# Performance work log

Hardware: AMD Instinct MI355X
Metric: run time of the kernel (lower is better)

Reference implementation:

```python
import jax, jax.numpy as jnp
import numpy as np

N_NODES = 50000
N_EDGES = 800000
D = 128
L = 3


def setup_inputs() -> dict:
    key = jax.random.key(0)
    ks = jax.random.split(key, 8)
    h = jax.random.normal(ks[0], (N_NODES, D), dtype=jnp.float32)
    src = jax.random.randint(ks[1], (N_EDGES,), 0, N_NODES, dtype=jnp.int32)
    dst = jax.random.randint(ks[2], (N_EDGES,), 0, N_NODES, dtype=jnp.int32)
    # MLP weights per GIN layer, scaled ~Glorot to keep activations bounded across layers
    w_scale = 0.05
    W1 = jax.random.normal(ks[3], (L, D, D), dtype=jnp.float32) * w_scale
    b1 = jnp.zeros((L, D), dtype=jnp.float32)
    W2 = jax.random.normal(ks[4], (L, D, D), dtype=jnp.float32) * w_scale
    b2 = jnp.zeros((L, D), dtype=jnp.float32)
    eps = jnp.zeros((L,), dtype=jnp.float32)  # init_eps=0, learnable
    return {"h": h, "src": src, "dst": dst, "W1": W1, "b1": b1, "W2": W2, "b2": b2, "eps": eps}


def reference(h, src, dst, W1, b1, W2, b2, eps):
    # GIN: h <- MLP((1 + eps) * h + sum_{(u->v) in E} h_u) per layer (sum aggregation)
    n = h.shape[0]
    for l in range(W1.shape[0]):
        agg = jax.ops.segment_sum(h[src], dst, num_segments=n)  # [N, D]
        z = (1.0 + eps[l]) * h + agg
        hid = jnp.maximum(z @ W1[l] + b1[l], 0.0)  # Linear + ReLU
        h = hid @ W2[l] + b2[l]                    # Linear
    return h
```

## Files before the change

kernel.cpp:

```cpp
#include <hip/hip_runtime.h>
#include <hip/hip_bf16.h>
#include <stdint.h>

#define N_NODES 50000
#define N_EDGES 800000
#define D 128
#define NLAYER 3
#define NGROUP (N_NODES / 16)
#define CAPG 384
#define GSTRIDE 384
#define MAXCH 12

#define NBKT2 196
#define BCAP 4608
#define EPB_A 2048
#define PA_BLOCKS ((N_EDGES + EPB_A - 1) / EPB_A)

typedef __attribute__((ext_vector_type(8))) short bf16x8;
typedef __attribute__((ext_vector_type(4))) float f32x4;
typedef __attribute__((ext_vector_type(2))) float f32x2;

__device__ __forceinline__ short f2bf(float f) {
    union { float f; uint32_t u; } v; v.f = f;
    uint32_t u = v.u;
    uint32_t r = u + 0x7fffu + ((u >> 16) & 1u);
    return (short)(r >> 16);
}
__device__ __forceinline__ float bf2f(short s) {
    union { uint32_t u; float f; } v;
    v.u = ((uint32_t)(uint16_t)s) << 16;
    return v.f;
}

__device__ __forceinline__ bf16x8 f8_to_bf16x8(uint2 r) {
    f32x2 f01 = __builtin_amdgcn_cvt_pk_f32_fp8(r.x, false);
    f32x2 f23 = __builtin_amdgcn_cvt_pk_f32_fp8(r.x, true);
    f32x2 f45 = __builtin_amdgcn_cvt_pk_f32_fp8(r.y, false);
    f32x2 f67 = __builtin_amdgcn_cvt_pk_f32_fp8(r.y, true);
    uint32_t w0, w1, w2, w3;
    asm("v_cvt_pk_bf16_f32 %0, %1, %2" : "=v"(w0) : "v"(f01.x), "v"(f01.y));
    asm("v_cvt_pk_bf16_f32 %0, %1, %2" : "=v"(w1) : "v"(f23.x), "v"(f23.y));
    asm("v_cvt_pk_bf16_f32 %0, %1, %2" : "=v"(w2) : "v"(f45.x), "v"(f45.y));
    asm("v_cvt_pk_bf16_f32 %0, %1, %2" : "=v"(w3) : "v"(f67.x), "v"(f67.y));
    union { uint32_t w[4]; bf16x8 v; } u;
    u.w[0] = w0; u.w[1] = w1; u.w[2] = w2; u.w[3] = w3;
    return u.v;
}

__device__ __forceinline__ unsigned char f2fp8(float f) {
    return (unsigned char)(__builtin_amdgcn_cvt_pk_fp8_f32(f, f, 0u, false) & 0xFF);
}

__global__ void wconv(const float* __restrict__ W1, const float* __restrict__ W2,
                      short* __restrict__ Wswz) {
    int t = blockIdx.x * blockDim.x + threadIdx.x;
    if (t >= NLAYER * 2 * 4 * 8 * 64) return;
    int lane = t & 63;
    int nt   = (t >> 6) & 7;
    int ks   = (t >> 9) & 3;
    int mat  = (t >> 11) & 1;
    int l    = t >> 12;
    const float* W = (mat == 0 ? W1 : W2) + (size_t)l * D * D;
    int n = nt * 16 + (lane & 15);
    short* outp = Wswz + (size_t)t * 8;
#pragma unroll
    for (int j = 0; j < 8; ++j) {
        int k = ks * 32 + (lane >> 4) * 8 + j;
        outp[j] = f2bf(W[k * D + n]);
    }
}

__global__ void h2bf(const float* __restrict__ h, short* __restrict__ hbf,
                     unsigned char* __restrict__ hf8) {
    int t = blockIdx.x * blockDim.x + threadIdx.x;
    if (t >= N_NODES * D / 8) return;
    f32x4 a = ((const f32x4*)h)[2 * t];
    f32x4 b = ((const f32x4*)h)[2 * t + 1];
    bf16x8 o;
    o[0] = f2bf(a.x); o[1] = f2bf(a.y); o[2] = f2bf(a.z); o[3] = f2bf(a.w);
    o[4] = f2bf(b.x); o[5] = f2bf(b.y); o[6] = f2bf(b.z); o[7] = f2bf(b.w);
    ((bf16x8*)hbf)[t] = o;
    uint32_t lo = 0, hi = 0;
    lo = __builtin_amdgcn_cvt_pk_fp8_f32(a.x, a.y, lo, false);
    lo = __builtin_amdgcn_cvt_pk_fp8_f32(a.z, a.w, lo, true);
    hi = __builtin_amdgcn_cvt_pk_fp8_f32(b.x, b.y, hi, false);
    hi = __builtin_amdgcn_cvt_pk_fp8_f32(b.z, b.w, hi, true);
    ((uint2*)hf8)[t] = make_uint2(lo, hi);
}

__global__ void zero_bcur(int* __restrict__ bcur) {
    if (threadIdx.x < NBKT2) bcur[threadIdx.x] = 0;
}

__global__ __launch_bounds__(256) void packA(const int* __restrict__ src,
                                             const int* __restrict__ dst,
                                             int* __restrict__ bcur,
                                             int* __restrict__ epack) {
    __shared__ int hcnt[NBKT2];
    __shared__ int hbase[NBKT2];
    if (threadIdx.x < NBKT2) hcnt[threadIdx.x] = 0;
    __syncthreads();
    int base = blockIdx.x * EPB_A;
    int end = base + EPB_A; if (end > N_EDGES) end = N_EDGES;
    for (int e = base + threadIdx.x; e < end; e += 256)
        atomicAdd(&hcnt[dst[e] >> 8], 1);
    __syncthreads();
    if (threadIdx.x < NBKT2) {
        int c = hcnt[threadIdx.x];
        hbase[threadIdx.x] = c ? atomicAdd(&bcur[threadIdx.x], c) : 0;
        hcnt[threadIdx.x] = 0;
    }
    __syncthreads();
    for (int e = base + threadIdx.x; e < end; e += 256) {
        int s = src[e], d = dst[e];
        int b = d >> 8;
        int r = atomicAdd(&hcnt[b], 1);
        int slot = hbase[b] + r;
        if (slot < BCAP)
            epack[(size_t)b * BCAP + slot] = (s << 8) | (d & 255);
    }
}

__global__ __launch_bounds__(256) void segB(const int* __restrict__ epack,
                                            const int* __restrict__ bcur,
                                            int* __restrict__ esd,
                                            int* __restrict__ gcnt) {
    __shared__ int image[16 * GSTRIDE];
    __shared__ int cur[16];
    const int b = blockIdx.x;
    int n = bcur[b]; if (n > BCAP) n = BCAP;
    const int* ep = epack + (size_t)b * BCAP;
    const int nG = (NGROUP - b * 16 < 16) ? (NGROUP - b * 16) : 16;

    for (int i = threadIdx.x; i < 16 * GSTRIDE; i += 256) image[i] = 0x80;
    if (threadIdx.x < 16) cur[threadIdx.x] = 0;
    __syncthreads();
    for (int i = threadIdx.x; i < n; i += 256) {
        int e = ep[i];
        int g = (e >> 4) & 15;
        int r = atomicAdd(&cur[g], 1);
        if (r < CAPG) image[g * GSTRIDE + r] = e & ~0xF0;
    }
    __syncthreads();
    if (threadIdx.x < nG) {
        int c = cur[threadIdx.x];
        gcnt[b * 16 + threadIdx.x] = (c > CAPG) ? CAPG : c;
    }
    for (int i = threadIdx.x; i < nG * GSTRIDE; i += 256)
        esd[(size_t)(b * 16) * GSTRIDE + i] = image[i];
}

__global__ __launch_bounds__(256) void gin_layer(const short* __restrict__ hbf,
                                                 const unsigned char* __restrict__ hf8,
                                                 const int* __restrict__ gcnt,
                                                 const int* __restrict__ esd,
                                                 const short* __restrict__ Wl,
                                                 const float* __restrict__ b1,
                                                 const float* __restrict__ b2,
                                                 const float* __restrict__ eps, int l,
                                                 float* __restrict__ outf,
                                                 short* __restrict__ outbf,
                                                 unsigned char* __restrict__ outf8,
                                                 int last) {
    __shared__ union {
        short stg[2][4096];
        struct { short zl[2048]; short hl[2048]; } t;
    } sm;
    __shared__ __align__(8) unsigned char dmask[512];

    const int lane = threadIdx.x & 63;
    const int wid  = threadIdx.x >> 6;
    const int g    = blockIdx.x;
    const int n0   = g * 16;
    const int m    = lane & 15;
    const int kh   = lane >> 4;

    const int lo  = g * GSTRIDE;
    int cnt = gcnt[g]; if (cnt > CAPG) cnt = CAPG;
    const int nch = (cnt + 31) >> 5;
    const uint32_t one = 0x3F80u;

    const int sl  = lane >> 2;
    const int wq8 = wid * 32 + (lane & 3) * 8;

    const uint32_t stg_base =
        (uint32_t)(uintptr_t)(__attribute__((address_space(3))) short*)&sm.stg[0][0];

    f32x4 acc[2];
    acc[0] = (f32x4)(0.0f); acc[1] = (f32x4)(0.0f);

    const int* ep = esd + lo;

    int esvA[MAXCH], esvB[MAXCH];
#pragma unroll
    for (int c = 0; c < MAXCH; ++c) {
        esvA[c] = ep[c * 32 + sl];
        esvB[c] = ep[c * 32 + 16 + sl];
    }

#define LDPAIR(rA, rB, c) do { \
        rA = *(const uint2*)(hf8 + (((uint32_t)(esvA[(c)] & ~0xFF)) >> 1) + wq8); \
        rB = *(const uint2*)(hf8 + (((uint32_t)(esvB[(c)] & ~0xFF)) >> 1) + wq8); \
    } while (0)

    auto cw = [&](int b, uint2 rA, uint2 rB) {
        short* base = &sm.stg[b][0] + wid * 1024 + lane * 8;
        *(bf16x8*)base         = f8_to_bf16x8(rA);
        *(bf16x8*)(base + 512) = f8_to_bf16x8(rB);
    };

    uint2 rA0, rB0, rA1, rB1;
    LDPAIR(rA0, rB0, 0);
    LDPAIR(rA1, rB1, 1);

    if (wid == 0 && (lane & 3) == 0) {
        const int sA = sl, sB = 16 + sl;
        const int pA = ((sA >> 1) & 3) * 8 + 2 * (sA >> 3) + (sA & 1);
        const int pB = ((sB >> 1) & 3) * 8 + 2 * (sB >> 3) + (sB & 1);
#pragma unroll
        for (int c = 0; c < MAXCH; ++c) {
            dmask[c * 32 + pA] = (unsigned char)(esvA[c] & 0xFF);
            dmask[c * 32 + pB] = (unsigned char)(esvB[c] & 0xFF);
        }
    }
    asm volatile("s_waitcnt lgkmcnt(0)" ::: "memory");
    __builtin_amdgcn_s_barrier();

    cw(0, rA0, rB0);

#pragma unroll
    for (int c = 0; c < MAXCH; ++c) {
        if (c >= nch) break;
        if (c + 2 < MAXCH) {
            if (c & 1) LDPAIR(rA1, rB1, c + 2);
            else       LDPAIR(rA0, rB0, c + 2);
        }
        if (c + 1 < nch) {
            if ((c + 1) & 1) cw(1, rA1, rB1);
            else             cw(0, rA0, rB0);
        }

        uint32_t breg = stg_base + (uint32_t)((c & 1) * 8192 + wid * 2048) + lane * 8;
        uint64_t t0, t1, t2, t3;
        asm volatile("ds_read_b64_tr_b16 %0, %1"             : "=v"(t0) : "v"(breg));
        asm volatile("ds_read_b64_tr_b16 %0, %1 offset:512"  : "=v"(t1) : "v"(breg));
        asm volatile("ds_read_b64_tr_b16 %0, %1 offset:1024" : "=v"(t2) : "v"(breg));
        asm volatile("ds_read_b64_tr_b16 %0, %1 offset:1536" : "=v"(t3) : "v"(breg));
        uint2 dm = *(const uint2*)&dmask[c * 32 + kh * 8];
        asm volatile("s_waitcnt lgkmcnt(0)" ::: "memory");
        __builtin_amdgcn_sched_barrier(0);

        union U64 { uint64_t u; uint32_t d[2]; };
        U64 p0, p1, p2, p3; p0.u = t0; p1.u = t1; p2.u = t2; p3.u = t3;
        union { uint32_t w[4]; bf16x8 v; } bf0, bf1;
        bf0.w[0] = (p0.d[0] & 0xFFFFu) | (p0.d[1] << 16);
        bf1.w[0] = (p0.d[0] >> 16) | (p0.d[1] & 0xFFFF0000u);
        bf0.w[1] = (p1.d[0] & 0xFFFFu) | (p1.d[1] << 16);
        bf1.w[1] = (p1.d[0] >> 16) | (p1.d[1] & 0xFFFF0000u);
        bf0.w[2] = (p2.d[0] & 0xFFFFu) | (p2.d[1] << 16);
        bf1.w[2] = (p2.d[0] >> 16) | (p2.d[1] & 0xFFFF0000u);
        bf0.w[3] = (p3.d[0] & 0xFFFFu) | (p3.d[1] << 16);
        bf1.w[3] = (p3.d[0] >> 16) | (p3.d[1] & 0xFFFF0000u);

        bf16x8 am;
#pragma unroll
        for (int e = 0; e < 4; ++e) {
            am[e]     = (((dm.x >> (e * 8)) & 255u) == (uint32_t)m) ? (short)one : (short)0;
            am[e + 4] = (((dm.y >> (e * 8)) & 255u) == (uint32_t)m) ? (short)one : (short)0;
        }
        acc[0] = __builtin_amdgcn_mfma_f32_16x16x32_bf16(am, bf0.v, acc[0], 0, 0, 0);
        acc[1] = __builtin_amdgcn_mfma_f32_16x16x32_bf16(am, bf1.v, acc[1], 0, 0, 0);
    }

    {
        const float se = 1.0f + eps[l];
#pragma unroll
        for (int t = 0; t < 2; ++t) {
            int col = (wid * 2 + t) * 16 + m;
#pragma unroll
            for (int r = 0; r < 4; ++r) {
                int row = n0 + kh * 4 + r;
                acc[t][r] += se * bf2f(hbf[(size_t)row * D + col]);
            }
        }
    }

    __syncthreads();

#pragma unroll
    for (int t = 0; t < 2; ++t) {
        int col = (wid * 2 + t) * 16 + m;
        int gi = col >> 3, ci = col & 7;
#pragma unroll
        for (int r = 0; r < 4; ++r) {
            int row = kh * 4 + r;
            sm.t.zl[row * 128 + ((gi ^ (row & 7)) << 3) + ci] = f2bf(acc[t][r]);
        }
    }
    __syncthreads();

    f32x4 acc1[2];
    acc1[0] = (f32x4)(0.0f); acc1[1] = (f32x4)(0.0f);
#pragma unroll
    for (int ks = 0; ks < 4; ++ks) {
        int gidx = ks * 4 + kh;
        bf16x8 af = *(const bf16x8*)&sm.t.zl[m * 128 + ((gidx ^ (m & 7)) * 8)];
#pragma unroll
        for (int t = 0; t < 2; ++t) {
            int nt = wid * 2 + t;
            bf16x8 bf = *(const bf16x8*)(Wl + ((size_t)(ks * 8 + nt) * 64 + lane) * 8);
            acc1[t] = __builtin_amdgcn_mfma_f32_16x16x32_bf16(af, bf, acc1[t], 0, 0, 0);
        }
    }
#pragma unroll
    for (int t = 0; t < 2; ++t) {
        int col = (wid * 2 + t) * 16 + m;
        float bias = b1[col];
#pragma unroll
        for (int r = 0; r < 4; ++r) {
            int hrow = kh * 4 + r;
            float v = fmaxf(acc1[t][r] + bias, 0.0f);
            sm.t.hl[hrow * 128 + (col ^ ((hrow & 7) << 3))] = f2bf(v);
        }
    }
    __syncthreads();

    f32x4 acc2[2];
    acc2[0] = (f32x4)(0.0f); acc2[1] = (f32x4)(0.0f);
    const short* W2p = Wl + 4 * 8 * 64 * 8;
#pragma unroll
    for (int ks = 0; ks < 4; ++ks) {
        int c0 = ks * 32 + kh * 8;
        bf16x8 af = *(const bf16x8*)&sm.t.hl[m * 128 + (c0 ^ ((m & 7) << 3))];
#pragma unroll
        for (int t = 0; t < 2; ++t) {
            int nt = wid * 2 + t;
            bf16x8 bf = *(const bf16x8*)(W2p + ((size_t)(ks * 8 + nt) * 64 + lane) * 8);
            acc2[t] = __builtin_amdgcn_mfma_f32_16x16x32_bf16(af, bf, acc2[t], 0, 0, 0);
        }
    }
#pragma unroll
    for (int t = 0; t < 2; ++t) {
        int col = (wid * 2 + t) * 16 + m;
        float bias = b2[col];
#pragma unroll
        for (int r = 0; r < 4; ++r) {
            int orow = n0 + kh * 4 + r;
            float v = acc2[t][r] + bias;
            if (last) {
                outf[(size_t)orow * D + col] = v;
            } else {
                outbf[(size_t)orow * D + col] = f2bf(v);
                outf8[(size_t)orow * D + col] = f2fp8(v);
            }
        }
    }
#undef LDPAIR
}

extern "C" void kernel_launch(void* const* d_in, const int* in_sizes, int n_in,
                              void* d_out, int out_size, void* d_ws, size_t ws_size,
                              hipStream_t stream) {
    const float* h   = (const float*)d_in[0];
    const int*   src = (const int*)d_in[1];
    const int*   dst = (const int*)d_in[2];
    const float* W1  = (const float*)d_in[3];
    const float* b1  = (const float*)d_in[4];
    const float* W2  = (const float*)d_in[5];
    const float* b2  = (const float*)d_in[6];
    const float* eps = (const float*)d_in[7];
    float* out = (float*)d_out;

    char* ws = (char*)d_ws;
    const size_t MB = 1024 * 1024;
    short* hbfA = (short*)ws;
    short* hbfB = (short*)(ws + 13 * MB);
    unsigned char* hf8A = (unsigned char*)(ws + 26 * MB);
    unsigned char* hf8B = (unsigned char*)(ws + 33 * MB);
    short* Wswz = (short*)(ws + 40 * MB);
    int*   gcnt = (int*)(ws + 40 * MB + 512 * 1024);
    int*   bcur = (int*)(ws + 40 * MB + 768 * 1024);
    int*   esd  = (int*)(ws + 41 * MB);
    int*   epack= (int*)(ws + 46 * MB);

    wconv<<<48, 256, 0, stream>>>(W1, W2, Wswz);
    h2bf<<<(N_NODES * D / 8 + 255) / 256, 256, 0, stream>>>(h, hbfA, hf8A);
    zero_bcur<<<1, 256, 0, stream>>>(bcur);
    packA<<<PA_BLOCKS, 256, 0, stream>>>(src, dst, bcur, epack);
    segB<<<NBKT2, 256, 0, stream>>>(epack, bcur, esd, gcnt);

    const short*         hin[3]  = {hbfA, hbfB, hbfA};
    const unsigned char* f8in[3] = {hf8A, hf8B, hf8A};
    short*         houtbf[3] = {hbfB, hbfA, nullptr};
    unsigned char* houtf8[3] = {hf8B, hf8A, nullptr};

    for (int l = 0; l < NLAYER; ++l) {
        gin_layer<<<NGROUP, 256, 0, stream>>>(hin[l], f8in[l], gcnt, esd,
                                              Wswz + (size_t)l * 2 * 16384,
                                              b1 + (size_t)l * D, b2 + (size_t)l * D,
                                              eps, l, out, houtbf[l], houtf8[l],
                                              l == NLAYER - 1 ? 1 : 0);
    }
}
```

Baseline: 143.3 us.

## Deepen gather prefetch to three stages and remap gather lanes per wave

The edge-gather loop now keeps three chunks of fp8 neighbor rows in flight in a register ring instead of two, using explicit vmcnt waits. Each staging-buffer write is followed by a barrier at the end of the iteration. The lane mapping also changes: each wave now gathers whole 128-byte rows for its own set of edge slots and scatters them into the shared-memory layout, and every wave writes part of the destination mask. The aim is to hide more gather latency and make the global loads more coalesced, at the cost of extra registers and a block barrier on every chunk.

```diff
diff --git a/kernel.cpp b/kernel.cpp
--- a/kernel.cpp
+++ b/kernel.cpp
@@ -180,8 +180,9 @@
     const int nch = (cnt + 31) >> 5;
     const uint32_t one = 0x3F80u;
 
-    const int sl  = lane >> 2;
-    const int wq8 = wid * 32 + (lane & 3) * 8;
+    const int sA   = wid * 4 + (lane >> 4);
+    const int rq8  = (lane & 15) * 8;
+    const int wdst = ((lane & 15) >> 2) * 1024 + sA * 32 + (lane & 3) * 8;
 
     const uint32_t stg_base =
         (uint32_t)(uintptr_t)(__attribute__((address_space(3))) short*)&sm.stg[0][0];
@@ -194,28 +195,29 @@
     int esvA[MAXCH], esvB[MAXCH];
 #pragma unroll
     for (int c = 0; c < MAXCH; ++c) {
-        esvA[c] = ep[c * 32 + sl];
-        esvB[c] = ep[c * 32 + 16 + sl];
-    }
-
-#define LDPAIR(rA, rB, c) do { \
-        rA = *(const uint2*)(hf8 + (((uint32_t)(esvA[(c)] & ~0xFF)) >> 1) + wq8); \
-        rB = *(const uint2*)(hf8 + (((uint32_t)(esvB[(c)] & ~0xFF)) >> 1) + wq8); \
+        esvA[c] = ep[c * 32 + sA];
+        esvB[c] = ep[c * 32 + 16 + sA];
+    }
+
+    uint2 rA[3], rB[3];
+#define LDPAIR(s, c) do { \
+        rA[(s)] = *(const uint2*)(hf8 + (((uint32_t)(esvA[(c)] & ~0xFF)) >> 1) + rq8); \
+        rB[(s)] = *(const uint2*)(hf8 + (((uint32_t)(esvB[(c)] & ~0xFF)) >> 1) + rq8); \
     } while (0)
 
-    auto cw = [&](int b, uint2 rA, uint2 rB) {
-        short* base = &sm.stg[b][0] + wid * 1024 + lane * 8;
-        *(bf16x8*)base         = f8_to_bf16x8(rA);
-        *(bf16x8*)(base + 512) = f8_to_bf16x8(rB);
+    auto cw = [&](int b, uint2 ra, uint2 rb) {
+        short* base = &sm.stg[b][0] + wdst;
+        *(bf16x8*)base         = f8_to_bf16x8(ra);
+        *(bf16x8*)(base + 512) = f8_to_bf16x8(rb);
     };
 
-    uint2 rA0, rB0, rA1, rB1;
-    LDPAIR(rA0, rB0, 0);
-    LDPAIR(rA1, rB1, 1);
-
-    if (wid == 0 && (lane & 3) == 0) {
-        const int sA = sl, sB = 16 + sl;
+    LDPAIR(0, 0);
+    LDPAIR(1, 1);
+    LDPAIR(2, 2);
+
+    if ((lane & 15) == 0) {
         const int pA = ((sA >> 1) & 3) * 8 + 2 * (sA >> 3) + (sA & 1);
+        const int sB = 16 + sA;
         const int pB = ((sB >> 1) & 3) * 8 + 2 * (sB >> 3) + (sB & 1);
 #pragma unroll
         for (int c = 0; c < MAXCH; ++c) {
@@ -223,22 +225,15 @@
             dmask[c * 32 + pB] = (unsigned char)(esvB[c] & 0xFF);
         }
     }
+    asm volatile("s_waitcnt vmcnt(4)" ::: "memory");
+    cw(0, rA[0], rB[0]);
     asm volatile("s_waitcnt lgkmcnt(0)" ::: "memory");
     __builtin_amdgcn_s_barrier();
 
-    cw(0, rA0, rB0);
-
 #pragma unroll
     for (int c = 0; c < MAXCH; ++c) {
         if (c >= nch) break;
-        if (c + 2 < MAXCH) {
-            if (c & 1) LDPAIR(rA1, rB1, c + 2);
-            else       LDPAIR(rA0, rB0, c + 2);
-        }
-        if (c + 1 < nch) {
-            if ((c + 1) & 1) cw(1, rA1, rB1);
-            else             cw(0, rA0, rB0);
-        }
+        if (c + 3 < nch) LDPAIR(c % 3, c + 3);
 
         uint32_t breg = stg_base + (uint32_t)((c & 1) * 8192 + wid * 2048) + lane * 8;
         uint64_t t0, t1, t2, t3;
@@ -270,6 +265,15 @@
         }
         acc[0] = __builtin_amdgcn_mfma_f32_16x16x32_bf16(am, bf0.v, acc[0], 0, 0, 0);
         acc[1] = __builtin_amdgcn_mfma_f32_16x16x32_bf16(am, bf1.v, acc[1], 0, 0, 0);
+
+        if (c + 1 < nch) {
+            if (c + 3 < nch)      asm volatile("s_waitcnt vmcnt(4)" ::: "memory");
+            else if (c + 2 < nch) asm volatile("s_waitcnt vmcnt(2)" ::: "memory");
+            else                  asm volatile("s_waitcnt vmcnt(0)" ::: "memory");
+            cw((c + 1) & 1, rA[(c + 1) % 3], rB[(c + 1) % 3]);
+            asm volatile("s_waitcnt lgkmcnt(0)" ::: "memory");
+            __builtin_amdgcn_s_barrier();
+        }
     }
 
     {
```

Measured after the change: 211.9 us. +47.8%, slower.
